# Optimization experiments

Measured on AMD Instinct MI355X. Metric: run time of the kernel, lower is better.

The kernel has to match this reference:

```python
import jax, jax.numpy as jnp
import numpy as np

B, F0, D = 4096, 39, 16
CIN = [128, 128, 128]


def setup_inputs() -> dict:
    key = jax.random.key(0)
    ks = jax.random.split(key, 4)
    x = jax.random.normal(ks[0], (B, F0, D), dtype=jnp.float32)
    fields = [F0] + CIN
    inp = {"embedded_features": x}
    for i in range(len(CIN)):
        cin = F0 * fields[i]
        cout = fields[i + 1]
        kw = jax.random.fold_in(ks[1], i)
        # Conv1d default init scale ~ 1/sqrt(fan_in)
        inp[f"W{i}"] = jax.random.normal(kw, (cout, cin), dtype=jnp.float32) / np.sqrt(cin)
        inp[f"b{i}"] = jnp.zeros((cout,), dtype=jnp.float32)
    return inp


def _cin_layer(X0, Xi, W, b):
    # Math identical to: outer_product [B,F0,Fi,D] -> reshape [B,F0*Fi,D] -> 1x1 Conv1d.
    # Conv1d(kernel=1) over the flattened F0*Fi channel dim is a contraction over (j,k):
    #   Xn[b,h,d] = sum_{j,k} W[h, j*Fi+k] * X0[b,j,d] * Xi[b,k,d] + b[h]
    H = W.shape[0]
    F0_, Fi = X0.shape[1], Xi.shape[1]
    Wr = W.reshape(H, F0_, Fi)
    return jnp.einsum('hjk,bjd,bkd->bhd', Wr, X0, Xi) + b[None, :, None]


def reference(embedded_features, W0, b0, W1, b1, W2, b2):
    X0 = embedded_features  # [B, F0, D]
    Ws = [(W0, b0), (W1, b1), (W2, b2)]
    Xi = X0
    res = []
    for W, b in Ws:
        Xi = _cin_layer(X0, Xi, W, b)  # [B, H_i, D]
        res.append(Xi.sum(axis=2))     # sum over embedding dim
    return jnp.concatenate(res, axis=1)  # [B, sum(cin_size)]
```

## Files before the change

kernel.cpp:

```cpp
#include <hip/hip_runtime.h>
#include <stdint.h>


#define NB_F0 39
#define NB_H  128
#define NB_B  4096

typedef float f32x4  __attribute__((ext_vector_type(4)));
typedef float f32x16 __attribute__((ext_vector_type(16)));
typedef short s16x8  __attribute__((ext_vector_type(8)));

__device__ __forceinline__ unsigned short rne_bf16(float f) {
  union { float f; unsigned u; } v; v.f = f;
  return (unsigned short)((v.u + 0x7fffu + ((v.u >> 16) & 1u)) >> 16);
}
__device__ __forceinline__ float bf16_to_f32(unsigned short s) {
  union { unsigned u; float f; } v; v.u = ((unsigned)s) << 16;
  return v.f;
}

__global__ void prep_x0_kernel(const float* __restrict__ X0g,
                               unsigned short* __restrict__ X0T,
                               float* __restrict__ X0f) {
  const int b = blockIdx.x;
  const int t = threadIdx.x;
  {
    const int d  = t >> 4;
    const int k4 = (t & 15) << 2;
    unsigned short vv[4];
#pragma unroll
    for (int i = 0; i < 4; ++i) {
      const int k = k4 + i;
      vv[i] = (k < NB_F0) ? rne_bf16(X0g[(size_t)b * (NB_F0 * 16) + k * 16 + d])
                          : (unsigned short)0;
    }
    ushort4 pk; pk.x = vv[0]; pk.y = vv[1]; pk.z = vv[2]; pk.w = vv[3];
    *(ushort4*)&X0T[((size_t)b * 16 + d) * 64 + k4] = pk;
  }
  for (int idx = t; idx < NB_F0 * 16; idx += 256)
    X0f[(size_t)b * (NB_F0 * 16) + idx] =
        bf16_to_f32(rne_bf16(X0g[(size_t)b * (NB_F0 * 16) + idx]));
}

__global__ void prep_w_kernel(const float* __restrict__ Wsrc,
                              unsigned short* __restrict__ Wdst,
                              int Fi, int kshift, int total) {
  int idx = blockIdx.x * 256 + threadIdx.x;
  if (idx >= total) return;
  const int i    = idx & 7;
  const int lane = (idx >> 3) & 63;
  const int c    = (idx >> 9) & ((1 << kshift) - 1);
  const int jt   = idx >> (9 + kshift);
  const int t    = jt & 3;
  const int j    = jt >> 2;
  const int h = t * 32 + (lane & 31);
  const int k = c * 16 + ((lane >> 5) << 3) + i;
  unsigned short v = 0;
  if (k < Fi) v = rne_bf16(Wsrc[(size_t)h * (NB_F0 * Fi) + j * Fi + k]);
  Wdst[idx] = v;
}

template <int FI_PAD, bool STORE_XN>
__global__ __launch_bounds__(256, 3) void cin_layer(
    const unsigned short* __restrict__ Wf,
    const unsigned short* __restrict__ XiT,
    const float* __restrict__ X0f,
    const float* __restrict__ bias,
    unsigned short* __restrict__ XnT,
    float* __restrict__ outp)
{
  constexpr int KPASS = FI_PAD / 64;
  constexpr int KC16  = FI_PAD / 16;
  constexpr int S     = NB_F0 * KPASS;

  __shared__ __attribute__((aligned(16))) float x0s[8 * NB_F0 * 16];

  const int tid  = threadIdx.x;
  const int lane = tid & 63;
  const int wv   = tid >> 6;
  const int L    = lane >> 5;
  const int col  = lane & 31;
  const int ht   = blockIdx.x >> 9;
  const int bblk = (blockIdx.x & 511) * 8;
  const int bwave = bblk + wv * 2;

  {
    const f32x4* src = (const f32x4*)(X0f + (size_t)bblk * (NB_F0 * 16));
    f32x4* dst = (f32x4*)x0s;
    for (int c = tid; c < (8 * NB_F0 * 16) / 4; c += 256) dst[c] = src[c];
  }
  __syncthreads();

  s16x8 af[4];
  auto load_af = [&](int pass) {
    const unsigned short* base = XiT +
        ((size_t)(bwave + (col >> 4)) * 16 + (col & 15)) * FI_PAD + pass * 64 + L * 8;
#pragma unroll
    for (int c = 0; c < 4; ++c) af[c] = *(const s16x8*)(base + c * 16);
  };
  load_af(0);

  const unsigned short* wbase = Wf + ((size_t)ht * KC16) * 512 + lane * 8;
  auto wload = [&](int s, s16x8* dst) {
    const int pass = (KPASS == 2 && s >= NB_F0) ? 1 : 0;
    const int j = s - pass * NB_F0;
    const unsigned short* p = wbase + ((size_t)j * 4 * KC16 + pass * 4) * 512;
#pragma unroll
    for (int c = 0; c < 4; ++c) dst[c] = *(const s16x8*)(p + c * 512);
  };

  f32x16 Xacc, kZero;
#pragma unroll
  for (int r = 0; r < 16; ++r) { Xacc[r] = 0.f; kZero[r] = 0.f; }

  auto stage = [&](int s, const s16x8* wfr) {
    const int j = (KPASS == 2 && s >= NB_F0) ? s - NB_F0 : s;
    f32x16 y;
    y = __builtin_amdgcn_mfma_f32_32x32x16_bf16(af[0], wfr[0], kZero, 0, 0, 0);
    y = __builtin_amdgcn_mfma_f32_32x32x16_bf16(af[1], wfr[1], y, 0, 0, 0);
    y = __builtin_amdgcn_mfma_f32_32x32x16_bf16(af[2], wfr[2], y, 0, 0, 0);
    y = __builtin_amdgcn_mfma_f32_32x32x16_bf16(af[3], wfr[3], y, 0, 0, 0);
    const float* xb = &x0s[((wv * 2) * NB_F0 + j) * 16 + 4 * L];
    const f32x4 x00 = *(const f32x4*)(xb);
    const f32x4 x01 = *(const f32x4*)(xb + 8);
    const f32x4 x10 = *(const f32x4*)(xb + NB_F0 * 16);
    const f32x4 x11 = *(const f32x4*)(xb + NB_F0 * 16 + 8);
#pragma unroll
    for (int r = 0; r < 4; ++r) {
      Xacc[r]      += x00[r] * y[r];
      Xacc[r + 4]  += x01[r] * y[r + 4];
      Xacc[r + 8]  += x10[r] * y[r + 8];
      Xacc[r + 12] += x11[r] * y[r + 12];
    }
  };

  s16x8 wfA[4], wfB[4];
  wload(0, wfA);
  for (int s = 0; s + 1 < S; s += 2) {
    wload(s + 1, wfB);
    stage(s, wfA);
    if (s + 2 < S) wload(s + 2, wfA);
    if (KPASS == 2 && s + 1 == NB_F0) load_af(1);
    stage(s + 1, wfB);
  }
  if (S & 1) stage(S - 1, wfA);

  const float bias_v = bias[ht * 32 + col];
  if (STORE_XN) {
#pragma unroll
    for (int r = 0; r < 16; ++r) {
      const int bp = r >> 3;
      const int d  = (r & 3) + 8 * ((r >> 2) & 1) + 4 * L;
      XnT[((size_t)(bwave + bp) * 16 + d) * NB_H + ht * 32 + col] =
          rne_bf16(Xacc[r] + bias_v);
    }
  }
  float s0 = 8.f * bias_v, s1 = 8.f * bias_v;
#pragma unroll
  for (int r = 0; r < 8; ++r) { s0 += Xacc[r]; s1 += Xacc[r + 8]; }
  s0 += __shfl_xor(s0, 32);
  s1 += __shfl_xor(s1, 32);
  if (lane < 32) {
    outp[(size_t)bwave * 384 + ht * 32 + lane] = s0;
    outp[(size_t)(bwave + 1) * 384 + ht * 32 + lane] = s1;
  }
}

extern "C" void kernel_launch(void* const* d_in, const int* in_sizes, int n_in,
                              void* d_out, int out_size, void* d_ws, size_t ws_size,
                              hipStream_t stream) {
  (void)in_sizes; (void)n_in; (void)out_size; (void)ws_size;
  const float* X0g = (const float*)d_in[0];
  const float* W0  = (const float*)d_in[1];
  const float* b0  = (const float*)d_in[2];
  const float* W1  = (const float*)d_in[3];
  const float* b1  = (const float*)d_in[4];
  const float* W2  = (const float*)d_in[5];
  const float* b2  = (const float*)d_in[6];
  float* out = (float*)d_out;

  char* p = (char*)d_ws;
  unsigned short* X0T = (unsigned short*)p; p += (size_t)NB_B * 16 * 64 * 2;
  float*          X0f = (float*)p;          p += (size_t)NB_B * NB_F0 * 16 * 4;
  unsigned short* X1T = (unsigned short*)p; p += (size_t)NB_B * 16 * 128 * 2;
  unsigned short* X2T = (unsigned short*)p; p += (size_t)NB_B * 16 * 128 * 2;
  unsigned short* Wf0 = (unsigned short*)p; p += (size_t)NB_F0 * 4 * 4 * 512 * 2;
  unsigned short* Wf1 = (unsigned short*)p; p += (size_t)NB_F0 * 4 * 8 * 512 * 2;
  unsigned short* Wf2 = (unsigned short*)p; p += (size_t)NB_F0 * 4 * 8 * 512 * 2;

  hipLaunchKernelGGL(prep_x0_kernel, dim3(NB_B), dim3(256), 0, stream,
                     X0g, X0T, X0f);
  const int tw0  = NB_F0 * 4 * 4 * 512;
  const int tw12 = NB_F0 * 4 * 8 * 512;
  hipLaunchKernelGGL(prep_w_kernel, dim3((tw0 + 255) / 256), dim3(256), 0, stream,
                     W0, Wf0, 39, 2, tw0);
  hipLaunchKernelGGL(prep_w_kernel, dim3((tw12 + 255) / 256), dim3(256), 0, stream,
                     W1, Wf1, 128, 3, tw12);
  hipLaunchKernelGGL(prep_w_kernel, dim3((tw12 + 255) / 256), dim3(256), 0, stream,
                     W2, Wf2, 128, 3, tw12);

  hipLaunchKernelGGL((cin_layer<64, true>),   dim3(2048), dim3(256), 0, stream,
                     Wf0, X0T, X0f, b0, X1T, out + 0);
  hipLaunchKernelGGL((cin_layer<128, true>),  dim3(2048), dim3(256), 0, stream,
                     Wf1, X1T, X0f, b1, X2T, out + 128);
  hipLaunchKernelGGL((cin_layer<128, false>), dim3(2048), dim3(256), 0, stream,
                     Wf2, X2T, X0f, b2, (unsigned short*)nullptr, out + 256);
}
```

Before: 338.4 us.

## Share weight fragments across waves via LDS DMA and double per-wave batch tile

Weight fragments are now staged once per block into a double-buffered LDS area using global_load_lds DMA, instead of every wave loading all four fragments from global memory. Each wave now handles four batch rows (two MFMA chains sharing the weight operand), and the grid is halved. X0 is stored as bf16 in a permuted layout so that each lane reads 8 contiguous values with one load. The aim is to cut redundant weight traffic and improve MFMA reuse, at the cost of a __syncthreads per stage, higher register pressure and fewer blocks.

```diff
diff --git a/kernel.cpp b/kernel.cpp
--- a/kernel.cpp
+++ b/kernel.cpp
@@ -10,6 +10,12 @@
 typedef float f32x16 __attribute__((ext_vector_type(16)));
 typedef short s16x8  __attribute__((ext_vector_type(8)));
 
+__device__ __forceinline__ void dma16(const void* g, void* l) {
+  __builtin_amdgcn_global_load_lds(
+      (const __attribute__((address_space(1))) unsigned int*)g,
+      (__attribute__((address_space(3))) unsigned int*)l, 16, 0, 0);
+}
+
 __device__ __forceinline__ unsigned short rne_bf16(float f) {
   union { float f; unsigned u; } v; v.f = f;
   return (unsigned short)((v.u + 0x7fffu + ((v.u >> 16) & 1u)) >> 16);
@@ -21,7 +27,7 @@
 
 __global__ void prep_x0_kernel(const float* __restrict__ X0g,
                                unsigned short* __restrict__ X0T,
-                               float* __restrict__ X0f) {
+                               unsigned short* __restrict__ X0c) {
   const int b = blockIdx.x;
   const int t = threadIdx.x;
   {
@@ -37,9 +43,12 @@
     ushort4 pk; pk.x = vv[0]; pk.y = vv[1]; pk.z = vv[2]; pk.w = vv[3];
     *(ushort4*)&X0T[((size_t)b * 16 + d) * 64 + k4] = pk;
   }
-  for (int idx = t; idx < NB_F0 * 16; idx += 256)
-    X0f[(size_t)b * (NB_F0 * 16) + idx] =
-        bf16_to_f32(rne_bf16(X0g[(size_t)b * (NB_F0 * 16) + idx]));
+  for (int idx = t; idx < NB_F0 * 16; idx += 256) {
+    const int j = idx >> 4, pos = idx & 15;
+    const int d = (pos & 3) | (((pos >> 3) & 1) << 2) | (((pos >> 2) & 1) << 3);
+    X0c[(size_t)b * (NB_F0 * 16) + idx] =
+        rne_bf16(X0g[(size_t)b * (NB_F0 * 16) + j * 16 + d]);
+  }
 }
 
 __global__ void prep_w_kernel(const float* __restrict__ Wsrc,
@@ -64,7 +73,7 @@
 __global__ __launch_bounds__(256, 3) void cin_layer(
     const unsigned short* __restrict__ Wf,
     const unsigned short* __restrict__ XiT,
-    const float* __restrict__ X0f,
+    const unsigned short* __restrict__ X0c,
     const float* __restrict__ bias,
     unsigned short* __restrict__ XnT,
     float* __restrict__ outp)
@@ -73,96 +82,109 @@
   constexpr int KC16  = FI_PAD / 16;
   constexpr int S     = NB_F0 * KPASS;
 
-  __shared__ __attribute__((aligned(16))) float x0s[8 * NB_F0 * 16];
+  __shared__ __attribute__((aligned(16))) unsigned short Wlds[2][2048];
+  __shared__ __attribute__((aligned(16))) unsigned short x0s[16 * NB_F0 * 16];
 
   const int tid  = threadIdx.x;
   const int lane = tid & 63;
   const int wv   = tid >> 6;
   const int L    = lane >> 5;
   const int col  = lane & 31;
-  const int ht   = blockIdx.x >> 9;
-  const int bblk = (blockIdx.x & 511) * 8;
-  const int bwave = bblk + wv * 2;
+  const int ht   = blockIdx.x >> 8;
+  const int bblk = (blockIdx.x & 255) * 16;
+  const int bwave = bblk + wv * 4;
+
+  auto dma_stage = [&](int s, int buf) {
+    const int pass = (KPASS == 2 && s >= NB_F0) ? 1 : 0;
+    const int j = s - pass * NB_F0;
+    const unsigned short* src =
+        Wf + (((size_t)(j * 4 + ht) * KC16) + pass * 4 + wv) * 512 + lane * 8;
+    dma16(src, &Wlds[buf][wv * 512]);
+  };
 
   {
-    const f32x4* src = (const f32x4*)(X0f + (size_t)bblk * (NB_F0 * 16));
-    f32x4* dst = (f32x4*)x0s;
-    for (int c = tid; c < (8 * NB_F0 * 16) / 4; c += 256) dst[c] = src[c];
-  }
-  __syncthreads();
-
-  s16x8 af[4];
+    const unsigned short* src = X0c + (size_t)bblk * (NB_F0 * 16);
+    for (int c = tid; c < (16 * NB_F0 * 16) / 8; c += 256)
+      *(s16x8*)&x0s[c * 8] = *(const s16x8*)&src[c * 8];
+  }
+  dma_stage(0, 0);
+
+  s16x8 af[2][4];
   auto load_af = [&](int pass) {
-    const unsigned short* base = XiT +
-        ((size_t)(bwave + (col >> 4)) * 16 + (col & 15)) * FI_PAD + pass * 64 + L * 8;
-#pragma unroll
-    for (int c = 0; c < 4; ++c) af[c] = *(const s16x8*)(base + c * 16);
+#pragma unroll
+    for (int P = 0; P < 2; ++P) {
+      const unsigned short* base = XiT +
+          ((size_t)(bwave + 2 * P + (col >> 4)) * 16 + (col & 15)) * FI_PAD +
+          pass * 64 + L * 8;
+#pragma unroll
+      for (int c = 0; c < 4; ++c) af[P][c] = *(const s16x8*)(base + c * 16);
+    }
   };
   load_af(0);
 
-  const unsigned short* wbase = Wf + ((size_t)ht * KC16) * 512 + lane * 8;
-  auto wload = [&](int s, s16x8* dst) {
-    const int pass = (KPASS == 2 && s >= NB_F0) ? 1 : 0;
-    const int j = s - pass * NB_F0;
-    const unsigned short* p = wbase + ((size_t)j * 4 * KC16 + pass * 4) * 512;
-#pragma unroll
-    for (int c = 0; c < 4; ++c) dst[c] = *(const s16x8*)(p + c * 512);
-  };
-
-  f32x16 Xacc, kZero;
-#pragma unroll
-  for (int r = 0; r < 16; ++r) { Xacc[r] = 0.f; kZero[r] = 0.f; }
-
-  auto stage = [&](int s, const s16x8* wfr) {
+  f32x16 Xacc[2], kZero;
+#pragma unroll
+  for (int r = 0; r < 16; ++r) { Xacc[0][r] = 0.f; Xacc[1][r] = 0.f; kZero[r] = 0.f; }
+
+  const int x0base = (wv * 4) * (NB_F0 * 16) + L * 8;
+
+  for (int s = 0; s < S; ++s) {
+    __syncthreads();
+    if (s + 1 < S) dma_stage(s + 1, (s + 1) & 1);
+    if (KPASS == 2 && s == NB_F0) load_af(1);
+
     const int j = (KPASS == 2 && s >= NB_F0) ? s - NB_F0 : s;
-    f32x16 y;
-    y = __builtin_amdgcn_mfma_f32_32x32x16_bf16(af[0], wfr[0], kZero, 0, 0, 0);
-    y = __builtin_amdgcn_mfma_f32_32x32x16_bf16(af[1], wfr[1], y, 0, 0, 0);
-    y = __builtin_amdgcn_mfma_f32_32x32x16_bf16(af[2], wfr[2], y, 0, 0, 0);
-    y = __builtin_amdgcn_mfma_f32_32x32x16_bf16(af[3], wfr[3], y, 0, 0, 0);
-    const float* xb = &x0s[((wv * 2) * NB_F0 + j) * 16 + 4 * L];
-    const f32x4 x00 = *(const f32x4*)(xb);
-    const f32x4 x01 = *(const f32x4*)(xb + 8);
-    const f32x4 x10 = *(const f32x4*)(xb + NB_F0 * 16);
-    const f32x4 x11 = *(const f32x4*)(xb + NB_F0 * 16 + 8);
-#pragma unroll
-    for (int r = 0; r < 4; ++r) {
-      Xacc[r]      += x00[r] * y[r];
-      Xacc[r + 4]  += x01[r] * y[r + 4];
-      Xacc[r + 8]  += x10[r] * y[r + 8];
-      Xacc[r + 12] += x11[r] * y[r + 12];
-    }
-  };
-
-  s16x8 wfA[4], wfB[4];
-  wload(0, wfA);
-  for (int s = 0; s + 1 < S; s += 2) {
-    wload(s + 1, wfB);
-    stage(s, wfA);
-    if (s + 2 < S) wload(s + 2, wfA);
-    if (KPASS == 2 && s + 1 == NB_F0) load_af(1);
-    stage(s + 1, wfB);
-  }
-  if (S & 1) stage(S - 1, wfA);
+    const unsigned short* wb = &Wlds[s & 1][lane * 8];
+    const s16x8 w0 = *(const s16x8*)(wb);
+    const s16x8 w1 = *(const s16x8*)(wb + 512);
+    const s16x8 w2 = *(const s16x8*)(wb + 1024);
+    const s16x8 w3 = *(const s16x8*)(wb + 1536);
+
+    f32x16 y0, y1;
+    y0 = __builtin_amdgcn_mfma_f32_32x32x16_bf16(af[0][0], w0, kZero, 0, 0, 0);
+    y1 = __builtin_amdgcn_mfma_f32_32x32x16_bf16(af[1][0], w0, kZero, 0, 0, 0);
+    y0 = __builtin_amdgcn_mfma_f32_32x32x16_bf16(af[0][1], w1, y0, 0, 0, 0);
+    y1 = __builtin_amdgcn_mfma_f32_32x32x16_bf16(af[1][1], w1, y1, 0, 0, 0);
+    y0 = __builtin_amdgcn_mfma_f32_32x32x16_bf16(af[0][2], w2, y0, 0, 0, 0);
+    y1 = __builtin_amdgcn_mfma_f32_32x32x16_bf16(af[1][2], w2, y1, 0, 0, 0);
+    y0 = __builtin_amdgcn_mfma_f32_32x32x16_bf16(af[0][3], w3, y0, 0, 0, 0);
+    y1 = __builtin_amdgcn_mfma_f32_32x32x16_bf16(af[1][3], w3, y1, 0, 0, 0);
+
+#pragma unroll
+    for (int P = 0; P < 2; ++P) {
+      const f32x16& y = (P == 0) ? y0 : y1;
+#pragma unroll
+      for (int bh = 0; bh < 2; ++bh) {
+        const s16x8 xu = *(const s16x8*)
+            &x0s[x0base + (2 * P + bh) * (NB_F0 * 16) + j * 16];
+#pragma unroll
+        for (int m = 0; m < 8; ++m)
+          Xacc[P][bh * 8 + m] +=
+              bf16_to_f32((unsigned short)xu[m]) * y[bh * 8 + m];
+      }
+    }
+  }
 
   const float bias_v = bias[ht * 32 + col];
-  if (STORE_XN) {
-#pragma unroll
-    for (int r = 0; r < 16; ++r) {
-      const int bp = r >> 3;
-      const int d  = (r & 3) + 8 * ((r >> 2) & 1) + 4 * L;
-      XnT[((size_t)(bwave + bp) * 16 + d) * NB_H + ht * 32 + col] =
-          rne_bf16(Xacc[r] + bias_v);
-    }
-  }
-  float s0 = 8.f * bias_v, s1 = 8.f * bias_v;
-#pragma unroll
-  for (int r = 0; r < 8; ++r) { s0 += Xacc[r]; s1 += Xacc[r + 8]; }
-  s0 += __shfl_xor(s0, 32);
-  s1 += __shfl_xor(s1, 32);
-  if (lane < 32) {
-    outp[(size_t)bwave * 384 + ht * 32 + lane] = s0;
-    outp[(size_t)(bwave + 1) * 384 + ht * 32 + lane] = s1;
+#pragma unroll
+  for (int P = 0; P < 2; ++P) {
+#pragma unroll
+    for (int bh = 0; bh < 2; ++bh) {
+      const int b = bwave + 2 * P + bh;
+      float v[8];
+#pragma unroll
+      for (int m = 0; m < 8; ++m) v[m] = Xacc[P][bh * 8 + m] + bias_v;
+      if (STORE_XN) {
+#pragma unroll
+        for (int m = 0; m < 8; ++m) {
+          const int d = (m & 3) + 8 * ((m >> 2) & 1) + 4 * L;
+          XnT[((size_t)b * 16 + d) * NB_H + ht * 32 + col] = rne_bf16(v[m]);
+        }
+      }
+      float tot = ((v[0] + v[1]) + (v[2] + v[3])) + ((v[4] + v[5]) + (v[6] + v[7]));
+      tot += __shfl_xor(tot, 32);
+      if (lane < 32) outp[(size_t)b * 384 + ht * 32 + lane] = tot;
+    }
   }
 }
 
@@ -181,7 +203,7 @@
 
   char* p = (char*)d_ws;
   unsigned short* X0T = (unsigned short*)p; p += (size_t)NB_B * 16 * 64 * 2;
-  float*          X0f = (float*)p;          p += (size_t)NB_B * NB_F0 * 16 * 4;
+  unsigned short* X0c = (unsigned short*)p; p += (size_t)NB_B * NB_F0 * 16 * 2;
   unsigned short* X1T = (unsigned short*)p; p += (size_t)NB_B * 16 * 128 * 2;
   unsigned short* X2T = (unsigned short*)p; p += (size_t)NB_B * 16 * 128 * 2;
   unsigned short* Wf0 = (unsigned short*)p; p += (size_t)NB_F0 * 4 * 4 * 512 * 2;
@@ -189,7 +211,7 @@
   unsigned short* Wf2 = (unsigned short*)p; p += (size_t)NB_F0 * 4 * 8 * 512 * 2;
 
   hipLaunchKernelGGL(prep_x0_kernel, dim3(NB_B), dim3(256), 0, stream,
-                     X0g, X0T, X0f);
+                     X0g, X0T, X0c);
   const int tw0  = NB_F0 * 4 * 4 * 512;
   const int tw12 = NB_F0 * 4 * 8 * 512;
   hipLaunchKernelGGL(prep_w_kernel, dim3((tw0 + 255) / 256), dim3(256), 0, stream,
@@ -199,10 +221,10 @@
   hipLaunchKernelGGL(prep_w_kernel, dim3((tw12 + 255) / 256), dim3(256), 0, stream,
                      W2, Wf2, 128, 3, tw12);
 
-  hipLaunchKernelGGL((cin_layer<64, true>),   dim3(2048), dim3(256), 0, stream,
-                     Wf0, X0T, X0f, b0, X1T, out + 0);
-  hipLaunchKernelGGL((cin_layer<128, true>),  dim3(2048), dim3(256), 0, stream,
-                     Wf1, X1T, X0f, b1, X2T, out + 128);
-  hipLaunchKernelGGL((cin_layer<128, false>), dim3(2048), dim3(256), 0, stream,
-                     Wf2, X2T, X0f, b2, (unsigned short*)nullptr, out + 256);
-}
+  hipLaunchKernelGGL((cin_layer<64, true>),   dim3(1024), dim3(256), 0, stream,
+                     Wf0, X0T, X0c, b0, X1T, out + 0);
+  hipLaunchKernelGGL((cin_layer<128, true>),  dim3(1024), dim3(256), 0, stream,
+                     Wf1, X1T, X0c, b1, X2T, out + 128);
+  hipLaunchKernelGGL((cin_layer<128, false>), dim3(1024), dim3(256), 0, stream,
+                     Wf2, X2T, X0c, b2, (unsigned short*)nullptr, out + 256);
+}
```

Result: faster. 328.3 us (-3.0%).
